# Kernel tuning notes

Measured on AMD Instinct MI355X. Metric: run time of the kernel, lower is better.

The kernel has to match this reference:

```python
import jax, jax.numpy as jnp
import numpy as np

EMBED = 512
HEADS = 8
DH = EMBED // HEADS  # 64
M = 256              # num_landmarks
ITERS = 6            # pinv iterations
SCALE = DH ** -0.5
RES_K = 33           # lucidrains residual_conv_kernel default


def _layer_norm(x, g, b, eps=1e-5):
    mu = jnp.mean(x, axis=-1, keepdims=True)
    var = jnp.mean((x - mu) ** 2, axis=-1, keepdims=True)
    return (x - mu) / jnp.sqrt(var + eps) * g + b


def _pinv_iter(x, iters=ITERS):
    # Moore-Penrose iterative pseudo-inverse (lucidrains nystrom-attention)
    abs_x = jnp.abs(x)
    denom = jnp.max(abs_x.sum(-1)) * jnp.max(abs_x.sum(-2))
    z = jnp.swapaxes(x, -1, -2) / denom
    I = jnp.eye(x.shape[-1], dtype=x.dtype)
    for _ in range(iters):
        xz = x @ z
        z = 0.25 * z @ (13 * I - xz @ (15 * I - xz @ (7 * I - xz)))
    return z


def _dwconv2d(x, w, b):
    # x: [B,C,H,W], w: [C,1,kh,kw] depthwise, SAME padding (odd kernels == k//2)
    out = jax.lax.conv_general_dilated(x, w, (1, 1), 'SAME',
                                       dimension_numbers=('NCHW', 'OIHW', 'NCHW'),
                                       feature_group_count=x.shape[1])
    return out + b[None, :, None, None]


def _nystrom_attn(x, Wqkv, Wo, bo, res_w):
    # x: [B, n, EMBED]; pad at FRONT so n divisible by M (matches F.pad(..., padding, 0) semantics)
    b, n, _ = x.shape
    pad = (M - n % M) % M
    x = jnp.pad(x, ((0, 0), (pad, 0), (0, 0)))
    npad = n + pad
    qkv = x @ Wqkv.T                               # [b, npad, 3*EMBED]
    q, k, v = jnp.split(qkv, 3, axis=-1)
    to_heads = lambda t: t.reshape(b, npad, HEADS, DH).transpose(0, 2, 1, 3)  # bhnd
    q, k, v = to_heads(q), to_heads(k), to_heads(v)
    q = q * SCALE
    l = npad // M
    q_land = q.reshape(b, HEADS, M, l, DH).mean(3)  # [b,h,M,d]
    k_land = k.reshape(b, HEADS, M, l, DH).mean(3)
    s1 = jnp.einsum('bhnd,bhmd->bhnm', q, k_land)
    s2 = jnp.einsum('bhmd,bhld->bhml', q_land, k_land)
    s3 = jnp.einsum('bhmd,bhnd->bhmn', q_land, k)
    a1 = jax.nn.softmax(s1, -1)
    a2 = jax.nn.softmax(s2, -1)
    a3 = jax.nn.softmax(s3, -1)
    a2_inv = _pinv_iter(a2)
    out = a1 @ (a2_inv @ (a3 @ v))                 # [b,h,npad,d]
    # residual depthwise conv over v: channels=heads, spatial=(npad, DH), kernel (33,1)
    res = jax.lax.conv_general_dilated(v, res_w, (1, 1), 'SAME',
                                       dimension_numbers=('NCHW', 'OIHW', 'NCHW'),
                                       feature_group_count=HEADS)
    out = out + res
    out = out.transpose(0, 2, 1, 3).reshape(b, npad, EMBED)
    out = out @ Wo.T + bo
    return out[:, -n:]                             # drop front padding


def setup_inputs() -> dict:
    key = jax.random.key(0)
    ks = jax.random.split(key, 32)
    s = 0.02
    inp = {}
    inp['data'] = jax.random.normal(ks[0], (4, 4096, 1536), jnp.float32)
    inp['W1'] = jax.random.normal(ks[1], (EMBED, 1536), jnp.float32) * s
    inp['b1'] = jnp.zeros((EMBED,), jnp.float32)
    inp['cls_token'] = jax.random.normal(ks[2], (1, 1, EMBED), jnp.float32)
    for li, base in ((1, 3), (2, 9)):
        inp[f'ln{li}_g'] = jnp.ones((EMBED,), jnp.float32)
        inp[f'ln{li}_b'] = jnp.zeros((EMBED,), jnp.float32)
        inp[f'Wqkv{li}'] = jax.random.normal(ks[base], (3 * EMBED, EMBED), jnp.float32) * s
        inp[f'Wo{li}'] = jax.random.normal(ks[base + 1], (EMBED, EMBED), jnp.float32) * s
        inp[f'bo{li}'] = jnp.zeros((EMBED,), jnp.float32)
        inp[f'res{li}'] = jax.random.normal(ks[base + 2], (HEADS, 1, RES_K, 1), jnp.float32) * s
    inp['pw7'] = jax.random.normal(ks[15], (EMBED, 1, 7, 7), jnp.float32) * s
    inp['pb7'] = jnp.zeros((EMBED,), jnp.float32)
    inp['pw5'] = jax.random.normal(ks[16], (EMBED, 1, 5, 5), jnp.float32) * s
    inp['pb5'] = jnp.zeros((EMBED,), jnp.float32)
    inp['pw3'] = jax.random.normal(ks[17], (EMBED, 1, 3, 3), jnp.float32) * s
    inp['pb3'] = jnp.zeros((EMBED,), jnp.float32)
    inp['lnf_g'] = jnp.ones((EMBED,), jnp.float32)
    inp['lnf_b'] = jnp.zeros((EMBED,), jnp.float32)
    inp['W2'] = jax.random.normal(ks[18], (2, EMBED), jnp.float32) * s
    inp['b2'] = jnp.zeros((2,), jnp.float32)
    return inp


def reference(data, W1, b1, cls_token, ln1_g, ln1_b, Wqkv1, Wo1, bo1, res1,
              ln2_g, ln2_b, Wqkv2, Wo2, bo2, res2,
              pw7, pb7, pw5, pb5, pw3, pb3, lnf_g, lnf_b, W2, b2):
    h = jax.nn.relu(data @ W1.T + b1)              # [B, N, EMBED]
    B, N, C = h.shape
    grid = int(np.ceil(np.sqrt(N)))
    add = grid * grid - N
    if add > 0:
        h = jnp.concatenate([h, h[:, :add]], axis=1)
    cls = jnp.broadcast_to(cls_token, (B, 1, C))
    h = jnp.concatenate([cls, h], axis=1)          # [B, 1+grid^2, C]
    # TransLayer 1
    h = h + _nystrom_attn(_layer_norm(h, ln1_g, ln1_b), Wqkv1, Wo1, bo1, res1)
    # PPEG
    cls_t, feat = h[:, :1], h[:, 1:]
    cnn = feat.transpose(0, 2, 1).reshape(B, C, grid, grid)
    x = _dwconv2d(cnn, pw7, pb7) + cnn + _dwconv2d(cnn, pw5, pb5) + _dwconv2d(cnn, pw3, pb3)
    feat = x.reshape(B, C, grid * grid).transpose(0, 2, 1)
    h = jnp.concatenate([cls_t, feat], axis=1)
    # TransLayer 2
    h = h + _nystrom_attn(_layer_norm(h, ln2_g, ln2_b), Wqkv2, Wo2, bo2, res2)
    h = _layer_norm(h, lnf_g, lnf_b)
    cls_feat = h[:, 0]
    logits = cls_feat @ W2.T + b2
    Y_prob = jax.nn.softmax(logits, -1)
    Y_hat = jnp.argmax(Y_prob, -1)
    return logits, Y_prob, Y_hat
```

## Files before the change

### kernel.cpp

```cpp
#include <hip/hip_runtime.h>
#include <math.h>

#define EMBED 512
#define HEADS 8
#define DH 64
#define MM 256
#define LSEG 17
#define NPAD 4352
#define NTOK 4097
#define N0 4096
#define BATCH 4
#define CIN 1536
#define QSCALE 0.125f
#define BH 32
#define NSEG 17

typedef float fp32x4 __attribute__((ext_vector_type(4)));
typedef short bf16x8 __attribute__((ext_vector_type(8)));
typedef short bf16x4 __attribute__((ext_vector_type(4)));
typedef unsigned short ushort_t;

__device__ __forceinline__ unsigned short f2bf(float f) {
  unsigned int u = __float_as_uint(f);
  u += 0x7fffu + ((u >> 16) & 1u);
  return (unsigned short)(u >> 16);
}
__device__ __forceinline__ float bf2f(unsigned short u) {
  return __uint_as_float((unsigned)u << 16);
}

__device__ __forceinline__ float block_sum(float v, float* red) {
  #pragma unroll
  for (int o = 1; o < 64; o <<= 1) v += __shfl_xor(v, o);
  int lane = threadIdx.x & 63, wid = threadIdx.x >> 6;
  if (lane == 0) red[wid] = v;
  __syncthreads();
  float r = red[0] + red[1] + red[2] + red[3];
  __syncthreads();
  return r;
}
__device__ __forceinline__ float block_max(float v, float* red) {
  #pragma unroll
  for (int o = 1; o < 64; o <<= 1) v = fmaxf(v, __shfl_xor(v, o));
  int lane = threadIdx.x & 63, wid = threadIdx.x >> 6;
  if (lane == 0) red[wid] = v;
  __syncthreads();
  float r = fmaxf(fmaxf(red[0], red[1]), fmaxf(red[2], red[3]));
  __syncthreads();
  return r;
}

__global__ __launch_bounds__(256) void gemm_abt(
    const float* __restrict__ A, const float* __restrict__ W,
    int Mrows, int Ncols, int K, const float* __restrict__ bias,
    float* __restrict__ out0, float* __restrict__ out1, float* __restrict__ out2,
    int mode)
{
  __shared__ unsigned short As[64][40];
  __shared__ unsigned short Ws[64][40];
  int tid = threadIdx.x;
  int lane = tid & 63;
  int wv = tid >> 6;
  int rowBase = blockIdx.y * 64, colBase = blockIdx.x * 64;
  int quad = lane >> 4;
  int l15 = lane & 15;
  int sr = tid >> 2;
  int skc = (tid & 3) * 8;

  fp32x4 acc[4] = {fp32x4{0,0,0,0}, fp32x4{0,0,0,0}, fp32x4{0,0,0,0}, fp32x4{0,0,0,0}};

  for (int kb = 0; kb < K; kb += 32) {
    __syncthreads();
    {
      int grow = rowBase + sr;
      float va[8];
      if (grow < Mrows) {
        const float4* p = (const float4*)&A[(size_t)grow * K + kb + skc];
        float4 v0 = p[0], v1 = p[1];
        va[0]=v0.x; va[1]=v0.y; va[2]=v0.z; va[3]=v0.w;
        va[4]=v1.x; va[5]=v1.y; va[6]=v1.z; va[7]=v1.w;
      } else {
        #pragma unroll
        for (int j = 0; j < 8; j++) va[j] = 0.f;
      }
      bf16x8 pk;
      #pragma unroll
      for (int j = 0; j < 8; j++) pk[j] = (short)f2bf(va[j]);
      *(bf16x8*)&As[sr][skc] = pk;
    }
    {
      int gcol = colBase + sr;
      const float4* p = (const float4*)&W[(size_t)gcol * K + kb + skc];
      float4 v0 = p[0], v1 = p[1];
      float vb[8] = {v0.x, v0.y, v0.z, v0.w, v1.x, v1.y, v1.z, v1.w};
      bf16x8 pk;
      #pragma unroll
      for (int j = 0; j < 8; j++) pk[j] = (short)f2bf(vb[j]);
      *(bf16x8*)&Ws[sr][skc] = pk;
    }
    __syncthreads();
    bf16x8 aF = *(const bf16x8*)&As[wv * 16 + l15][quad * 8];
    #pragma unroll
    for (int ns = 0; ns < 4; ns++) {
      bf16x8 bF = *(const bf16x8*)&Ws[ns * 16 + l15][quad * 8];
      acc[ns] = __builtin_amdgcn_mfma_f32_16x16x32_bf16(aF, bF, acc[ns], 0, 0, 0);
    }
  }

  #pragma unroll
  for (int ns = 0; ns < 4; ns++) {
    int col = colBase + ns * 16 + l15;
    #pragma unroll
    for (int i = 0; i < 4; i++) {
      int row = rowBase + wv * 16 + quad * 4 + i;
      if (row >= Mrows) continue;
      float v = acc[ns][i];
      if (mode == 0) {
        v += bias[col];
        v = fmaxf(v, 0.f);
        int b = row / N0, n = row % N0;
        out0[((size_t)b * NTOK + 1 + n) * EMBED + col] = v;
      } else if (mode == 1) {
        int b = row / NPAD, n = row % NPAD;
        int sec = col / EMBED;
        int hh = (col % EMBED) / DH;
        int d = col & 63;
        float* dst = (sec == 0) ? out0 : ((sec == 1) ? out1 : out2);
        if (sec == 0) v *= QSCALE;
        dst[(((size_t)b * HEADS + hh) * NPAD + n) * DH + d] = v;
      } else if (mode == 2) {
        v += bias[col];
        out0[(size_t)row * EMBED + col] += v;
      } else {
        v += bias[col];
        float full = out0[(size_t)row * EMBED + col] + v;
        out0[(size_t)row * EMBED + col] = full;
        int b = row / NTOK, t = row % NTOK;
        if (t > 0) out1[((size_t)b * N0 + (t - 1)) * EMBED + col] = full;
      }
    }
  }
}

#define BSWZ(n, k) ((((k) + (((n) >> 3) & 3) * 8)) & 31)
__global__ __launch_bounds__(256) void gemm_nn_bf16(
    const unsigned short* __restrict__ A, const unsigned short* __restrict__ B,
    unsigned short* __restrict__ C,
    int Nsize, float beta, float sgn, float gamma, int transOut)
{
  __shared__ unsigned short As[64][40];
  __shared__ unsigned short BsT[64][40];
  int batch = blockIdx.z;
  const unsigned short* Ab = A + (size_t)batch * MM * MM;
  const unsigned short* Bb = B + (size_t)batch * MM * Nsize;
  unsigned short* Cb = C + (size_t)batch * MM * Nsize;
  int tid = threadIdx.x;
  int lane = tid & 63, wv = tid >> 6, quad = lane >> 4, l15 = lane & 15;
  int rowBase = blockIdx.y * 64, colBase = blockIdx.x * 64;
  int asr = tid >> 2, ask = (tid & 3) * 8;
  int bkr = tid >> 3;
  int bnc = (tid & 7) * 8;
  fp32x4 acc[4] = {fp32x4{0,0,0,0}, fp32x4{0,0,0,0}, fp32x4{0,0,0,0}, fp32x4{0,0,0,0}};

  for (int kb = 0; kb < MM; kb += 32) {
    __syncthreads();
    *(bf16x8*)&As[asr][ask] =
        *(const bf16x8*)&Ab[(size_t)(rowBase + asr) * MM + kb + ask];
    {
      bf16x8 vb = *(const bf16x8*)&Bb[(size_t)(kb + bkr) * Nsize + colBase + bnc];
      #pragma unroll
      for (int j = 0; j < 8; j++) {
        int n = bnc + j;
        BsT[n][BSWZ(n, bkr)] = (unsigned short)vb[j];
      }
    }
    __syncthreads();
    bf16x8 aF = *(const bf16x8*)&As[wv * 16 + l15][quad * 8];
    #pragma unroll
    for (int ct = 0; ct < 4; ct++) {
      int n = ct * 16 + l15;
      bf16x8 bF = *(const bf16x8*)&BsT[n][BSWZ(n, quad * 8)];
      acc[ct] = __builtin_amdgcn_mfma_f32_16x16x32_bf16(aF, bF, acc[ct], 0, 0, 0);
    }
  }

  #pragma unroll
  for (int ct = 0; ct < 4; ct++) {
    int col = colBase + ct * 16 + l15;
    #pragma unroll
    for (int i = 0; i < 4; i++) {
      int row = rowBase + wv * 16 + quad * 4 + i;
      float v = sgn * acc[ct][i];
      if (beta != 0.f) v += beta * bf2f(Ab[(size_t)row * MM + col]);
      v *= gamma;
      if (transOut == 0) Cb[(size_t)row * Nsize + col] = f2bf(v);
      else               Cb[(size_t)col * MM + row] = f2bf(v);
    }
  }
}

__global__ void cls_kernel(const float* __restrict__ cls, float* __restrict__ h) {
  int t = blockIdx.x * blockDim.x + threadIdx.x;
  if (t >= BATCH * EMBED) return;
  int b = t / EMBED, c = t % EMBED;
  h[(size_t)b * NTOK * EMBED + c] = cls[c];
}

__global__ void zero_pad_kernel(float* __restrict__ xpad) {
  int t = blockIdx.x * blockDim.x + threadIdx.x;
  const int per = 255 * EMBED;
  if (t >= BATCH * per) return;
  int b = t / per, r = t % per;
  xpad[(size_t)b * NPAD * EMBED + r] = 0.f;
}

__global__ __launch_bounds__(256) void ln_pad_kernel(
    const float* __restrict__ h, const float* __restrict__ g,
    const float* __restrict__ be, float* __restrict__ xpad)
{
  __shared__ float red[4];
  int row = blockIdx.x;
  int b = row / NTOK, j = row % NTOK;
  const float* x = h + (size_t)row * EMBED;
  int tid = threadIdx.x;
  float v0 = x[tid], v1 = x[tid + 256];
  float mu = block_sum(v0 + v1, red) * (1.f / 512.f);
  float d0 = v0 - mu, d1 = v1 - mu;
  float var = block_sum(d0 * d0 + d1 * d1, red) * (1.f / 512.f);
  float inv = 1.f / sqrtf(var + 1e-5f);
  float* o = xpad + ((size_t)b * NPAD + 255 + j) * EMBED;
  o[tid]       = d0 * inv * g[tid]       + be[tid];
  o[tid + 256] = d1 * inv * g[tid + 256] + be[tid + 256];
}

__global__ __launch_bounds__(256) void landmarks_kernel(
    const float* __restrict__ q, const float* __restrict__ k,
    float* __restrict__ qland, float* __restrict__ kland)
{
  int bh = blockIdx.y;
  int m = blockIdx.x * 4 + (threadIdx.x >> 6);
  int d = threadIdx.x & 63;
  const float* qb = q + (size_t)bh * NPAD * DH;
  const float* kb = k + (size_t)bh * NPAD * DH;
  float sq = 0.f, sk = 0.f;
  int base = m * LSEG;
  #pragma unroll
  for (int t = 0; t < LSEG; t++) {
    sq += qb[(size_t)(base + t) * DH + d];
    sk += kb[(size_t)(base + t) * DH + d];
  }
  qland[((size_t)bh * MM + m) * DH + d] = sq * (1.f / LSEG);
  kland[((size_t)bh * MM + m) * DH + d] = sk * (1.f / LSEG);
}

__global__ __launch_bounds__(256) void s2_softmax_kernel(
    const float* __restrict__ qland, const float* __restrict__ kland,
    unsigned short* __restrict__ a2)
{
  __shared__ float qrow[64];
  __shared__ float red[4];
  int bh = blockIdx.y, m = blockIdx.x, tid = threadIdx.x;
  if (tid < 64) qrow[tid] = qland[((size_t)bh * MM + m) * DH + tid];
  __syncthreads();
  const float* kb = kland + (size_t)bh * MM * DH + (size_t)tid * DH;
  float s = 0.f;
  #pragma unroll 16
  for (int d = 0; d < 64; d++) s += qrow[d] * kb[d];
  float mx = block_max(s, red);
  float e = __expf(s - mx);
  float tot = block_sum(e, red);
  a2[((size_t)bh * MM + m) * MM + tid] = f2bf(e / tot);
}

__global__ void init_denom_kernel(float* __restrict__ denoms) {
  if (threadIdx.x < 2) denoms[threadIdx.x] = 0.f;
}

__global__ __launch_bounds__(256) void denom_kernel(
    const unsigned short* __restrict__ a2, float* __restrict__ denoms)
{
  __shared__ float red[4];
  int bh = blockIdx.x, tid = threadIdx.x;
  const unsigned short* A = a2 + (size_t)bh * MM * MM;
  float rs = 0.f, cs = 0.f;
  for (int j = 0; j < MM; j++) rs += bf2f(A[(size_t)tid * MM + j]);
  for (int i = 0; i < MM; i++) cs += bf2f(A[(size_t)i * MM + tid]);
  float mr = block_max(rs, red);
  float mc = block_max(cs, red);
  if (tid == 0) {
    atomicMax((int*)&denoms[0], __float_as_int(mr));
    atomicMax((int*)&denoms[1], __float_as_int(mc));
  }
}

__global__ void z0_kernel(const unsigned short* __restrict__ a2,
                          const float* __restrict__ denoms,
                          unsigned short* __restrict__ z)
{
  int bh = blockIdx.z;
  int i = blockIdx.y * 4 + threadIdx.y;
  int j = blockIdx.x * 64 + threadIdx.x;
  float denom = denoms[0] * denoms[1];
  z[((size_t)bh * MM + i) * MM + j] = f2bf(bf2f(a2[((size_t)bh * MM + j) * MM + i]) / denom);
}

__global__ __launch_bounds__(256) void a3v_part_mfma(
    const float* __restrict__ qland, const float* __restrict__ k,
    const float* __restrict__ v, float* __restrict__ Opart,
    float* __restrict__ mpart, float* __restrict__ lpart)
{
  __shared__ __align__(16) unsigned short qs[64][40];
  __shared__ __align__(16) unsigned short ks[256][72];
  __shared__ __align__(16) unsigned short vt[64][72];
  int tid = threadIdx.x;
  int lane = tid & 63, wv = tid >> 6, quad = lane >> 4, l15 = lane & 15;
  int bh = blockIdx.y;
  int ltile = blockIdx.x & 3;
  int seg = blockIdx.x >> 2;
  int l0 = ltile * 64;
  int key0 = seg * 256;
  const float* qb = qland + (size_t)bh * MM * DH;
  const float* kb = k + (size_t)bh * NPAD * DH;
  const float* vb = v + (size_t)bh * NPAD * DH;

  {
    int sr = tid >> 2, dc = (tid & 3) * 16;
    const float4* p = (const float4*)&qb[(size_t)(l0 + sr) * DH + dc];
    float4 v0 = p[0], v1 = p[1], v2 = p[2], v3 = p[3];
    float va[16] = {v0.x,v0.y,v0.z,v0.w, v1.x,v1.y,v1.z,v1.w,
                    v2.x,v2.y,v2.z,v2.w, v3.x,v3.y,v3.z,v3.w};
    bf16x8 p0, p1;
    #pragma unroll
    for (int j = 0; j < 8; j++) { p0[j] = (short)f2bf(va[j]); p1[j] = (short)f2bf(va[8 + j]); }
    *(bf16x8*)&qs[sr][dc] = p0;
    *(bf16x8*)&qs[sr][dc + 8] = p1;
  }
  #pragma unroll
  for (int i = 0; i < 16; i++) {
    int idx = i * 1024 + tid * 4;
    int r = idx >> 6, c = idx & 63;
    float4 vv = *(const float4*)&kb[(size_t)(key0 + r) * DH + c];
    bf16x4 pk = { (short)f2bf(vv.x), (short)f2bf(vv.y), (short)f2bf(vv.z), (short)f2bf(vv.w) };
    *(bf16x4*)&ks[r][c] = pk;
  }
  __syncthreads();

  fp32x4 sacc[16];
  #pragma unroll
  for (int ct = 0; ct < 16; ct++) sacc[ct] = fp32x4{0,0,0,0};
  bf16x8 aF0 = *(const bf16x8*)&qs[wv * 16 + l15][quad * 8];
  bf16x8 aF1 = *(const bf16x8*)&qs[wv * 16 + l15][32 + quad * 8];
  #pragma unroll
  for (int ct = 0; ct < 16; ct++) {
    bf16x8 b0 = *(const bf16x8*)&ks[ct * 16 + l15][quad * 8];
    bf16x8 b1 = *(const bf16x8*)&ks[ct * 16 + l15][32 + quad * 8];
    sacc[ct] = __builtin_amdgcn_mfma_f32_16x16x32_bf16(aF0, b0, sacc[ct], 0, 0, 0);
    sacc[ct] = __builtin_amdgcn_mfma_f32_16x16x32_bf16(aF1, b1, sacc[ct], 0, 0, 0);
  }

  float mrow[4], lrow[4];
  #pragma unroll
  for (int i = 0; i < 4; i++) {
    float m = -3.0e38f;
    #pragma unroll
    for (int ct = 0; ct < 16; ct++) m = fmaxf(m, sacc[ct][i]);
    #pragma unroll
    for (int o = 1; o < 16; o <<= 1) m = fmaxf(m, __shfl_xor(m, o));
    float s = 0.f;
    #pragma unroll
    for (int ct = 0; ct < 16; ct++) {
      float e = __expf(sacc[ct][i] - m);
      sacc[ct][i] = e;
      s += e;
    }
    #pragma unroll
    for (int o = 1; o < 16; o <<= 1) s += __shfl_xor(s, o);
    mrow[i] = m;
    lrow[i] = s;
  }
  __syncthreads();
  unsigned short* P = &ks[0][0];
  #pragma unroll
  for (int ct = 0; ct < 16; ct++)
    #pragma unroll
    for (int i = 0; i < 4; i++)
      P[(size_t)(wv * 16 + quad * 4 + i) * 264 + ct * 16 + l15] = f2bf(sacc[ct][i]);
  __syncthreads();

  fp32x4 oacc[4] = {fp32x4{0,0,0,0}, fp32x4{0,0,0,0}, fp32x4{0,0,0,0}, fp32x4{0,0,0,0}};
  int dh = tid & 63, kgrp = tid >> 6;
  for (int ch = 0; ch < 4; ch++) {
    if (ch) __syncthreads();
    {
      int kbase = kgrp * 16;
      #pragma unroll
      for (int g = 0; g < 4; g++) {
        short pk[4];
        #pragma unroll
        for (int r = 0; r < 4; r++)
          pk[r] = (short)f2bf(vb[(size_t)(key0 + ch * 64 + kbase + g * 4 + r) * DH + dh]);
        *(bf16x4*)&vt[dh][kbase + g * 4] = *(bf16x4*)pk;
      }
    }
    __syncthreads();
    #pragma unroll
    for (int ks2 = 0; ks2 < 2; ks2++) {
      bf16x8 aP = *(const bf16x8*)&P[(size_t)(wv * 16 + l15) * 264 + ch * 64 + ks2 * 32 + quad * 8];
      #pragma unroll
      for (int ct = 0; ct < 4; ct++) {
        bf16x8 bV = *(const bf16x8*)&vt[ct * 16 + l15][ks2 * 32 + quad * 8];
        oacc[ct] = __builtin_amdgcn_mfma_f32_16x16x32_bf16(aP, bV, oacc[ct], 0, 0, 0);
      }
    }
  }

  size_t base = ((size_t)seg * BH + bh) * MM + l0;
  #pragma unroll
  for (int ct = 0; ct < 4; ct++)
    #pragma unroll
    for (int i = 0; i < 4; i++) {
      int row = wv * 16 + quad * 4 + i;
      Opart[(base + row) * DH + ct * 16 + l15] = oacc[ct][i];
    }
  if (l15 == 0) {
    #pragma unroll
    for (int i = 0; i < 4; i++) {
      int row = wv * 16 + quad * 4 + i;
      mpart[base + row] = mrow[i];
      lpart[base + row] = lrow[i];
    }
  }
}

__global__ __launch_bounds__(256) void a3v_merge_kernel(
    const float* __restrict__ Opart, const float* __restrict__ mpart,
    const float* __restrict__ lpart, unsigned short* __restrict__ kv)
{
  int bh = blockIdx.y;
  int lbase = blockIdx.x * 64;
  int d = threadIdx.x & 63, lsub = threadIdx.x >> 6;
  for (int li = lsub; li < 64; li += 4) {
    int lm = lbase + li;
    float M = -3.0e38f;
    #pragma unroll
    for (int s = 0; s < NSEG; s++)
      M = fmaxf(M, mpart[((size_t)s * BH + bh) * MM + lm]);
    float L = 0.f, O = 0.f;
    #pragma unroll
    for (int s = 0; s < NSEG; s++) {
      size_t idx = ((size_t)s * BH + bh) * MM + lm;
      float w = __expf(mpart[idx] - M);
      L += lpart[idx] * w;
      O += Opart[idx * DH + d] * w;
    }
    kv[((size_t)bh * MM + lm) * DH + d] = f2bf(O / L);
  }
}

__global__ __launch_bounds__(256, 2) void attn1_mfma(
    const float* __restrict__ q, const float* __restrict__ kland,
    const unsigned short* __restrict__ kv2T, const float* __restrict__ v,
    const float* __restrict__ resw, float* __restrict__ attn)
{
  __shared__ __align__(16) unsigned short qs[64][40];
  __shared__ __align__(16) unsigned short klp[256][72];
  __shared__ __align__(16) unsigned short kvs[64][264];
  __shared__ float wsm[33];
  int tid = threadIdx.x;
  int lane = tid & 63, wv = tid >> 6, quad = lane >> 4, l15 = lane & 15;
  int bh = blockIdx.y, b = bh >> 3, hh = bh & 7;
  int n0 = 255 + blockIdx.x * 64;
  const float* qb  = q + (size_t)bh * NPAD * DH;
  const float* klb = kland + (size_t)bh * MM * DH;
  const unsigned short* kvb = kv2T + (size_t)bh * DH * MM;
  const float* vb  = v + (size_t)bh * NPAD * DH;
  if (tid < 33) wsm[tid] = resw[hh * 33 + tid];

  {
    int sr = tid >> 2, dc = (tid & 3) * 16;
    int g = n0 + sr; if (g > NPAD - 1) g = NPAD - 1;
    const float4* p = (const float4*)&qb[(size_t)g * DH + dc];
    float4 v0 = p[0], v1 = p[1], v2 = p[2], v3 = p[3];
    float va[16] = {v0.x,v0.y,v0.z,v0.w, v1.x,v1.y,v1.z,v1.w,
                    v2.x,v2.y,v2.z,v2.w, v3.x,v3.y,v3.z,v3.w};
    bf16x8 p0, p1;
    #pragma unroll
    for (int j = 0; j < 8; j++) { p0[j] = (short)f2bf(va[j]); p1[j] = (short)f2bf(va[8 + j]); }
    *(bf16x8*)&qs[sr][dc] = p0;
    *(bf16x8*)&qs[sr][dc + 8] = p1;
  }
  #pragma unroll
  for (int i = 0; i < 16; i++) {
    int idx = i * 1024 + tid * 4;
    int r = idx >> 6, c = idx & 63;
    float4 vv = *(const float4*)&klb[(size_t)r * DH + c];
    bf16x4 pk = { (short)f2bf(vv.x), (short)f2bf(vv.y), (short)f2bf(vv.z), (short)f2bf(vv.w) };
    *(bf16x4*)&klp[r][c] = pk;
  }
  #pragma unroll
  for (int i = 0; i < 8; i++) {
    int idx = i * 2048 + tid * 8;
    int r = idx >> 8, c = idx & 255;
    *(bf16x8*)&kvs[r][c] = *(const bf16x8*)&kvb[(size_t)r * MM + c];
  }
  __syncthreads();

  fp32x4 sacc[16];
  #pragma unroll
  for (int ct = 0; ct < 16; ct++) sacc[ct] = fp32x4{0,0,0,0};
  bf16x8 aF0 = *(const bf16x8*)&qs[wv * 16 + l15][quad * 8];
  bf16x8 aF1 = *(const bf16x8*)&qs[wv * 16 + l15][32 + quad * 8];
  #pragma unroll
  for (int ct = 0; ct < 16; ct++) {
    bf16x8 b0 = *(const bf16x8*)&klp[ct * 16 + l15][quad * 8];
    bf16x8 b1 = *(const bf16x8*)&klp[ct * 16 + l15][32 + quad * 8];
    sacc[ct] = __builtin_amdgcn_mfma_f32_16x16x32_bf16(aF0, b0, sacc[ct], 0, 0, 0);
    sacc[ct] = __builtin_amdgcn_mfma_f32_16x16x32_bf16(aF1, b1, sacc[ct], 0, 0, 0);
  }
  #pragma unroll
  for (int i = 0; i < 4; i++) {
    float m = -3.0e38f;
    #pragma unroll
    for (int ct = 0; ct < 16; ct++) m = fmaxf(m, sacc[ct][i]);
    #pragma unroll
    for (int o = 1; o < 16; o <<= 1) m = fmaxf(m, __shfl_xor(m, o));
    float s = 0.f;
    #pragma unroll
    for (int ct = 0; ct < 16; ct++) {
      float e = __expf(sacc[ct][i] - m);
      sacc[ct][i] = e;
      s += e;
    }
    #pragma unroll
    for (int o = 1; o < 16; o <<= 1) s += __shfl_xor(s, o);
    float inv = 1.f / s;
    #pragma unroll
    for (int ct = 0; ct < 16; ct++) sacc[ct][i] *= inv;
  }
  __syncthreads();
  unsigned short* P = &klp[0][0];
  #pragma unroll
  for (int ct = 0; ct < 16; ct++)
    #pragma unroll
    for (int i = 0; i < 4; i++)
      P[(size_t)(wv * 16 + quad * 4 + i) * 264 + ct * 16 + l15] = f2bf(sacc[ct][i]);
  __syncthreads();

  fp32x4 oacc[4] = {fp32x4{0,0,0,0}, fp32x4{0,0,0,0}, fp32x4{0,0,0,0}, fp32x4{0,0,0,0}};
  #pragma unroll
  for (int ks = 0; ks < 8; ks++) {
    bf16x8 aP = *(const bf16x8*)&P[(size_t)(wv * 16 + l15) * 264 + ks * 32 + quad * 8];
    #pragma unroll
    for (int ct = 0; ct < 4; ct++) {
      bf16x8 bV = *(const bf16x8*)&kvs[ct * 16 + l15][ks * 32 + quad * 8];
      oacc[ct] = __builtin_amdgcn_mfma_f32_16x16x32_bf16(aP, bV, oacc[ct], 0, 0, 0);
    }
  }
  __syncthreads();
  float* vwin = (float*)&kvs[0][0];
  #pragma unroll
  for (int i = 0; i < 6; i++) {
    int r = i * 16 + (tid >> 4), c = (tid & 15) * 4;
    int g = n0 - 16 + r;
    float4 vv;
    if (g <= NPAD - 1) vv = *(const float4*)&vb[(size_t)g * DH + c];
    else { vv.x = 0.f; vv.y = 0.f; vv.z = 0.f; vv.w = 0.f; }
    *(float4*)&vwin[r * 68 + c] = vv;
  }
  __syncthreads();
  #pragma unroll
  for (int ct = 0; ct < 4; ct++) {
    int c = ct * 16 + l15;
    #pragma unroll
    for (int i = 0; i < 4; i++) {
      int rl = wv * 16 + quad * 4 + i;
      int n = n0 + rl;
      if (n > NPAD - 1) continue;
      float ca = 0.f;
      #pragma unroll 11
      for (int t = 0; t < 33; t++) ca += vwin[(rl + t) * 68 + c] * wsm[t];
      attn[((size_t)b * NTOK + (n - 255)) * EMBED + hh * DH + c] = oacc[ct][i] + ca;
    }
  }
}

__global__ void prep_wcomb_kernel(
    const float* __restrict__ pw7, const float* __restrict__ pw5,
    const float* __restrict__ pw3, const float* __restrict__ pb7,
    const float* __restrict__ pb5, const float* __restrict__ pb3,
    float* __restrict__ wcomb, float* __restrict__ biasc)
{
  int i = blockIdx.x * blockDim.x + threadIdx.x;
  if (i < EMBED * 49) {
    int c = i / 49, tap = i % 49;
    int ky = tap / 7, kx = tap % 7;
    float v = pw7[c * 49 + tap];
    if (ky >= 1 && ky <= 5 && kx >= 1 && kx <= 5) v += pw5[c * 25 + (ky - 1) * 5 + (kx - 1)];
    if (ky >= 2 && ky <= 4 && kx >= 2 && kx <= 4) v += pw3[c * 9 + (ky - 2) * 3 + (kx - 2)];
    if (ky == 3 && kx == 3) v += 1.f;
    wcomb[tap * EMBED + c] = v;
  }
  if (i < EMBED) biasc[i] = pb7[i] + pb5[i] + pb3[i];
}

__global__ __launch_bounds__(256) void dwconv_kernel(
    const float* __restrict__ tmp, const float* __restrict__ wcomb,
    const float* __restrict__ biasc, float* __restrict__ h)
{
  __shared__ float4 wsm[49][32];
  int tx = threadIdx.x;
  int ty = threadIdx.y;
  int cb = blockIdx.x * 128;
  int c = cb + tx * 4;
  int b = blockIdx.z;
  int n = blockIdx.y * 8 + ty;
  int y = n >> 6, x = n & 63;
  int tid = ty * 32 + tx;
  for (int i = tid; i < 49 * 32; i += 256) {
    int tap = i >> 5, g = i & 31;
    wsm[tap][g] = *(const float4*)&wcomb[tap * EMBED + cb + g * 4];
  }
  __syncthreads();
  const float* src = tmp + (size_t)b * N0 * EMBED;
  float4 acc = *(const float4*)&biasc[c];
  #pragma unroll
  for (int ky = 0; ky < 7; ky++) {
    int yy = y + ky - 3;
    if (yy < 0 || yy >= 64) continue;
    #pragma unroll
    for (int kx = 0; kx < 7; kx++) {
      int xx = x + kx - 3;
      if (xx < 0 || xx >= 64) continue;
      float4 vv = *(const float4*)&src[((size_t)yy * 64 + xx) * EMBED + c];
      float4 w = wsm[ky * 7 + kx][tx];
      acc.x += vv.x * w.x;
      acc.y += vv.y * w.y;
      acc.z += vv.z * w.z;
      acc.w += vv.w * w.w;
    }
  }
  *(float4*)&h[((size_t)b * NTOK + 1 + n) * EMBED + c] = acc;
}

__global__ __launch_bounds__(256) void final_kernel(
    const float* __restrict__ h, const float* __restrict__ g,
    const float* __restrict__ be, const float* __restrict__ W2,
    const float* __restrict__ b2, float* __restrict__ out)
{
  __shared__ float red[4];
  int b = blockIdx.x, tid = threadIdx.x;
  const float* x = h + (size_t)b * NTOK * EMBED;
  float v0 = x[tid], v1 = x[tid + 256];
  float mu = block_sum(v0 + v1, red) * (1.f / 512.f);
  float d0 = v0 - mu, d1 = v1 - mu;
  float var = block_sum(d0 * d0 + d1 * d1, red) * (1.f / 512.f);
  float inv = 1.f / sqrtf(var + 1e-5f);
  float xn0 = d0 * inv * g[tid] + be[tid];
  float xn1 = d1 * inv * g[tid + 256] + be[tid + 256];
  float l0 = block_sum(xn0 * W2[tid] + xn1 * W2[tid + 256], red);
  float l1 = block_sum(xn0 * W2[512 + tid] + xn1 * W2[512 + tid + 256], red);
  if (tid == 0) {
    l0 += b2[0]; l1 += b2[1];
    out[b * 2 + 0] = l0;
    out[b * 2 + 1] = l1;
    float mx = fmaxf(l0, l1);
    float e0 = expf(l0 - mx), e1 = expf(l1 - mx);
    float s = e0 + e1;
    out[8 + b * 2 + 0] = e0 / s;
    out[8 + b * 2 + 1] = e1 / s;
    out[16 + b] = (l1 > l0) ? 1.f : 0.f;
  }
}

extern "C" void kernel_launch(void* const* d_in, const int* in_sizes, int n_in,
                              void* d_out, int out_size, void* d_ws, size_t ws_size,
                              hipStream_t stream)
{
  const float* data = (const float*)d_in[0];
  const float* W1   = (const float*)d_in[1];
  const float* b1   = (const float*)d_in[2];
  const float* cls  = (const float*)d_in[3];
  const float* lng[2]  = {(const float*)d_in[4],  (const float*)d_in[10]};
  const float* lnb[2]  = {(const float*)d_in[5],  (const float*)d_in[11]};
  const float* Wqkv[2] = {(const float*)d_in[6],  (const float*)d_in[12]};
  const float* Wo[2]   = {(const float*)d_in[7],  (const float*)d_in[13]};
  const float* bo[2]   = {(const float*)d_in[8],  (const float*)d_in[14]};
  const float* resw[2] = {(const float*)d_in[9],  (const float*)d_in[15]};
  const float* pw7 = (const float*)d_in[16];
  const float* pb7 = (const float*)d_in[17];
  const float* pw5 = (const float*)d_in[18];
  const float* pb5 = (const float*)d_in[19];
  const float* pw3 = (const float*)d_in[20];
  const float* pb3 = (const float*)d_in[21];
  const float* lnfg = (const float*)d_in[22];
  const float* lnfb = (const float*)d_in[23];
  const float* W2  = (const float*)d_in[24];
  const float* b2  = (const float*)d_in[25];

  float* ws = (float*)d_ws;
  size_t off = 0;
  auto alloc = [&](size_t n) { float* p = ws + off; off += n; return p; };
  float* hbuf  = alloc((size_t)BATCH * NTOK * EMBED);
  float* xpad  = alloc((size_t)BATCH * NPAD * EMBED);
  float* qbuf  = alloc((size_t)BH * NPAD * DH);
  float* kbuf  = alloc((size_t)BH * NPAD * DH);
  float* vbuf  = alloc((size_t)BH * NPAD * DH);
  float* qland = alloc((size_t)BH * MM * DH);
  float* kland = alloc((size_t)BH * MM * DH);
  float* a2f   = alloc((size_t)BH * MM * MM);
  float* za    = alloc((size_t)BH * MM * MM);
  float* zb    = alloc((size_t)BH * MM * MM);
  float* xzb   = alloc((size_t)BH * MM * MM);
  float* t1b   = alloc((size_t)BH * MM * MM);
  float* t2b   = alloc((size_t)BH * MM * MM);
  float* kvb   = alloc((size_t)BH * MM * DH);
  float* kv2b  = alloc((size_t)BH * MM * DH);
  float* wcomb = alloc(49 * EMBED);
  float* biasc = alloc(EMBED);
  float* denoms = alloc(64);
  float* mpart = alloc((size_t)NSEG * BH * MM);
  float* lpart = alloc((size_t)NSEG * BH * MM);
  float* attn = xpad;
  float* Opart = za;

  unsigned short* a2B  = (unsigned short*)a2f;
  unsigned short* zaB  = (unsigned short*)za;
  unsigned short* zbB  = (unsigned short*)zb;
  unsigned short* xzB  = (unsigned short*)xzb;
  unsigned short* t1B  = (unsigned short*)t1b;
  unsigned short* t2B  = (unsigned short*)t2b;
  unsigned short* kvB  = (unsigned short*)kvb;
  unsigned short* kv2B = (unsigned short*)kv2b;

  gemm_abt<<<dim3(EMBED / 64, (BATCH * N0) / 64), 256, 0, stream>>>(
      data, W1, BATCH * N0, EMBED, CIN, b1, hbuf, nullptr, nullptr, 0);
  cls_kernel<<<dim3((BATCH * EMBED + 255) / 256), 256, 0, stream>>>(cls, hbuf);

  for (int layer = 0; layer < 2; layer++) {
    ln_pad_kernel<<<dim3(BATCH * NTOK), 256, 0, stream>>>(hbuf, lng[layer], lnb[layer], xpad);
    zero_pad_kernel<<<dim3((BATCH * 255 * EMBED + 255) / 256), 256, 0, stream>>>(xpad);
    gemm_abt<<<dim3((3 * EMBED) / 64, (BATCH * NPAD) / 64), 256, 0, stream>>>(
        xpad, Wqkv[layer], BATCH * NPAD, 3 * EMBED, EMBED, nullptr, qbuf, kbuf, vbuf, 1);
    landmarks_kernel<<<dim3(MM / 4, BH), 256, 0, stream>>>(qbuf, kbuf, qland, kland);
    s2_softmax_kernel<<<dim3(MM, BH), 256, 0, stream>>>(qland, kland, a2B);
    init_denom_kernel<<<1, 64, 0, stream>>>(denoms);
    denom_kernel<<<dim3(BH), 256, 0, stream>>>(a2B, denoms);

    a3v_part_mfma<<<dim3(4 * NSEG, BH), 256, 0, stream>>>(
        qland, kbuf, vbuf, Opart, mpart, lpart);
    a3v_merge_kernel<<<dim3(MM / 64, BH), 256, 0, stream>>>(Opart, mpart, lpart, kvB);

    z0_kernel<<<dim3(MM / 64, MM / 4, BH), dim3(64, 4), 0, stream>>>(a2B, denoms, zaB);
    unsigned short* zin = zaB;
    unsigned short* zout = zbB;
    for (int it = 0; it < 6; it++) {
      gemm_nn_bf16<<<dim3(4, 4, BH), 256, 0, stream>>>(a2B, zin, xzB, MM, 0.f, 1.f, 1.f, 0);
      gemm_nn_bf16<<<dim3(4, 4, BH), 256, 0, stream>>>(xzB, xzB, t1B, MM, 7.f, -1.f, 1.f, 0);
      gemm_nn_bf16<<<dim3(4, 4, BH), 256, 0, stream>>>(xzB, t1B, t2B, MM, 15.f, -1.f, 1.f, 0);
      gemm_nn_bf16<<<dim3(4, 4, BH), 256, 0, stream>>>(zin, t2B, zout, MM, 13.f, -1.f, 0.25f, 0);
      unsigned short* t = zin; zin = zout; zout = t;
    }
    gemm_nn_bf16<<<dim3(1, 4, BH), 256, 0, stream>>>(zin, kvB, kv2B, DH, 0.f, 1.f, 1.f, 1);
    attn1_mfma<<<dim3((NTOK + 63) / 64, BH), 256, 0, stream>>>(
        qbuf, kland, kv2B, vbuf, resw[layer], attn);
    gemm_abt<<<dim3(EMBED / 64, (BATCH * NTOK + 63) / 64), 256, 0, stream>>>(
        attn, Wo[layer], BATCH * NTOK, EMBED, EMBED, bo[layer], hbuf,
        (layer == 0) ? qbuf : nullptr, nullptr, (layer == 0) ? 3 : 2);

    if (layer == 0) {
      prep_wcomb_kernel<<<dim3((EMBED * 49 + 255) / 256), 256, 0, stream>>>(
          pw7, pw5, pw3, pb7, pb5, pb3, wcomb, biasc);
      dwconv_kernel<<<dim3(EMBED / 128, N0 / 8, BATCH), dim3(32, 8), 0, stream>>>(
          qbuf, wcomb, biasc, hbuf);
    }
  }

  final_kernel<<<dim3(BATCH), 256, 0, stream>>>(hbuf, lnfg, lnfb, W2, b2, (float*)d_out);
}
```

Baseline: 1.703 ms.

## Store activations and weights in bf16, widen GEMM tiles, keep dual-layout pinv buffers

Converts the input data and weights to bf16 once up front, and stores q/k/v, the padded LN output, attention output and partial results as bf16 instead of fp32. This halves global memory traffic and removes the per-tile fp32-to-bf16 conversion inside the GEMMs. gemm_abt now computes 64x128 tiles. The pinv GEMMs write both row-major and column-major copies so B operands load without a transposing scatter into shared memory. The costs are extra conversion passes over the large input, doubled output writes in the pinv loop, and more bf16 rounding of intermediates.

After: 1.589 ms. -6.7%, faster.

```diff
diff --git a/kernel.cpp b/kernel.cpp
--- a/kernel.cpp
+++ b/kernel.cpp
@@ -18,7 +18,7 @@
 typedef float fp32x4 __attribute__((ext_vector_type(4)));
 typedef short bf16x8 __attribute__((ext_vector_type(8)));
 typedef short bf16x4 __attribute__((ext_vector_type(4)));
-typedef unsigned short ushort_t;
+typedef unsigned short u16;
 
 __device__ __forceinline__ unsigned short f2bf(float f) {
   unsigned int u = __float_as_uint(f);
@@ -50,136 +50,123 @@
   return r;
 }
 
+__global__ void f2bf_kernel(const float* __restrict__ in, u16* __restrict__ out, int n) {
+  int t = (blockIdx.x * 256 + threadIdx.x) * 8;
+  if (t >= n) return;
+  float4 a = *(const float4*)&in[t];
+  float4 b = *(const float4*)&in[t + 4];
+  bf16x8 pk;
+  pk[0]=(short)f2bf(a.x); pk[1]=(short)f2bf(a.y); pk[2]=(short)f2bf(a.z); pk[3]=(short)f2bf(a.w);
+  pk[4]=(short)f2bf(b.x); pk[5]=(short)f2bf(b.y); pk[6]=(short)f2bf(b.z); pk[7]=(short)f2bf(b.w);
+  *(bf16x8*)&out[t] = pk;
+}
+
 __global__ __launch_bounds__(256) void gemm_abt(
-    const float* __restrict__ A, const float* __restrict__ W,
+    const u16* __restrict__ A, const u16* __restrict__ W,
     int Mrows, int Ncols, int K, const float* __restrict__ bias,
-    float* __restrict__ out0, float* __restrict__ out1, float* __restrict__ out2,
+    float* __restrict__ fout, float* __restrict__ fout2,
+    u16* __restrict__ uo0, u16* __restrict__ uo1, u16* __restrict__ uo2,
     int mode)
 {
-  __shared__ unsigned short As[64][40];
-  __shared__ unsigned short Ws[64][40];
+  __shared__ u16 As[64][40];
+  __shared__ u16 Ws[128][40];
   int tid = threadIdx.x;
   int lane = tid & 63;
   int wv = tid >> 6;
-  int rowBase = blockIdx.y * 64, colBase = blockIdx.x * 64;
+  int rowBase = blockIdx.y * 64, colBase = blockIdx.x * 128;
   int quad = lane >> 4;
   int l15 = lane & 15;
   int sr = tid >> 2;
   int skc = (tid & 3) * 8;
 
-  fp32x4 acc[4] = {fp32x4{0,0,0,0}, fp32x4{0,0,0,0}, fp32x4{0,0,0,0}, fp32x4{0,0,0,0}};
+  fp32x4 acc[8];
+  #pragma unroll
+  for (int i = 0; i < 8; i++) acc[i] = fp32x4{0,0,0,0};
 
   for (int kb = 0; kb < K; kb += 32) {
     __syncthreads();
     {
       int grow = rowBase + sr;
-      float va[8];
-      if (grow < Mrows) {
-        const float4* p = (const float4*)&A[(size_t)grow * K + kb + skc];
-        float4 v0 = p[0], v1 = p[1];
-        va[0]=v0.x; va[1]=v0.y; va[2]=v0.z; va[3]=v0.w;
-        va[4]=v1.x; va[5]=v1.y; va[6]=v1.z; va[7]=v1.w;
-      } else {
-        #pragma unroll
-        for (int j = 0; j < 8; j++) va[j] = 0.f;
-      }
-      bf16x8 pk;
-      #pragma unroll
-      for (int j = 0; j < 8; j++) pk[j] = (short)f2bf(va[j]);
-      *(bf16x8*)&As[sr][skc] = pk;
-    }
-    {
-      int gcol = colBase + sr;
-      const float4* p = (const float4*)&W[(size_t)gcol * K + kb + skc];
-      float4 v0 = p[0], v1 = p[1];
-      float vb[8] = {v0.x, v0.y, v0.z, v0.w, v1.x, v1.y, v1.z, v1.w};
-      bf16x8 pk;
-      #pragma unroll
-      for (int j = 0; j < 8; j++) pk[j] = (short)f2bf(vb[j]);
-      *(bf16x8*)&Ws[sr][skc] = pk;
+      bf16x8 av;
+      if (grow < Mrows) av = *(const bf16x8*)&A[(size_t)grow * K + kb + skc];
+      else { bf16x8 z = {0,0,0,0,0,0,0,0}; av = z; }
+      *(bf16x8*)&As[sr][skc] = av;
+    }
+    #pragma unroll
+    for (int h = 0; h < 2; h++) {
+      int r = sr + h * 64;
+      *(bf16x8*)&Ws[r][skc] =
+          *(const bf16x8*)&W[(size_t)(colBase + r) * K + kb + skc];
     }
     __syncthreads();
     bf16x8 aF = *(const bf16x8*)&As[wv * 16 + l15][quad * 8];
     #pragma unroll
-    for (int ns = 0; ns < 4; ns++) {
-      bf16x8 bF = *(const bf16x8*)&Ws[ns * 16 + l15][quad * 8];
-      acc[ns] = __builtin_amdgcn_mfma_f32_16x16x32_bf16(aF, bF, acc[ns], 0, 0, 0);
-    }
-  }
-
-  #pragma unroll
-  for (int ns = 0; ns < 4; ns++) {
-    int col = colBase + ns * 16 + l15;
+    for (int ct = 0; ct < 8; ct++) {
+      bf16x8 bF = *(const bf16x8*)&Ws[ct * 16 + l15][quad * 8];
+      acc[ct] = __builtin_amdgcn_mfma_f32_16x16x32_bf16(aF, bF, acc[ct], 0, 0, 0);
+    }
+  }
+
+  #pragma unroll
+  for (int ct = 0; ct < 8; ct++) {
+    int col = colBase + ct * 16 + l15;
     #pragma unroll
     for (int i = 0; i < 4; i++) {
       int row = rowBase + wv * 16 + quad * 4 + i;
       if (row >= Mrows) continue;
-      float v = acc[ns][i];
+      float v = acc[ct][i];
       if (mode == 0) {
         v += bias[col];
         v = fmaxf(v, 0.f);
         int b = row / N0, n = row % N0;
-        out0[((size_t)b * NTOK + 1 + n) * EMBED + col] = v;
+        fout[((size_t)b * NTOK + 1 + n) * EMBED + col] = v;
       } else if (mode == 1) {
         int b = row / NPAD, n = row % NPAD;
         int sec = col / EMBED;
         int hh = (col % EMBED) / DH;
         int d = col & 63;
-        float* dst = (sec == 0) ? out0 : ((sec == 1) ? out1 : out2);
+        u16* dst = (sec == 0) ? uo0 : ((sec == 1) ? uo1 : uo2);
         if (sec == 0) v *= QSCALE;
-        dst[(((size_t)b * HEADS + hh) * NPAD + n) * DH + d] = v;
+        dst[(((size_t)b * HEADS + hh) * NPAD + n) * DH + d] = f2bf(v);
       } else if (mode == 2) {
         v += bias[col];
-        out0[(size_t)row * EMBED + col] += v;
+        fout[(size_t)row * EMBED + col] += v;
       } else {
         v += bias[col];
-        float full = out0[(size_t)row * EMBED + col] + v;
-        out0[(size_t)row * EMBED + col] = full;
+        float full = fout[(size_t)row * EMBED + col] + v;
+        fout[(size_t)row * EMBED + col] = full;
         int b = row / NTOK, t = row % NTOK;
-        if (t > 0) out1[((size_t)b * N0 + (t - 1)) * EMBED + col] = full;
+        if (t > 0) fout2[((size_t)b * N0 + (t - 1)) * EMBED + col] = full;
       }
     }
   }
 }
 
-#define BSWZ(n, k) ((((k) + (((n) >> 3) & 3) * 8)) & 31)
-__global__ __launch_bounds__(256) void gemm_nn_bf16(
-    const unsigned short* __restrict__ A, const unsigned short* __restrict__ B,
-    unsigned short* __restrict__ C,
-    int Nsize, float beta, float sgn, float gamma, int transOut)
-{
-  __shared__ unsigned short As[64][40];
-  __shared__ unsigned short BsT[64][40];
+__global__ __launch_bounds__(256) void gemm_nn2(
+    const u16* __restrict__ A, const u16* __restrict__ Bc,
+    u16* __restrict__ Cr, u16* __restrict__ Cc,
+    int Nsize, float beta, float sgn, float gamma)
+{
+  __shared__ u16 As[64][40];
+  __shared__ u16 Bs[64][40];
   int batch = blockIdx.z;
-  const unsigned short* Ab = A + (size_t)batch * MM * MM;
-  const unsigned short* Bb = B + (size_t)batch * MM * Nsize;
-  unsigned short* Cb = C + (size_t)batch * MM * Nsize;
+  const u16* Ab = A + (size_t)batch * MM * MM;
+  const u16* Bb = Bc + (size_t)batch * MM * Nsize;
   int tid = threadIdx.x;
   int lane = tid & 63, wv = tid >> 6, quad = lane >> 4, l15 = lane & 15;
   int rowBase = blockIdx.y * 64, colBase = blockIdx.x * 64;
-  int asr = tid >> 2, ask = (tid & 3) * 8;
-  int bkr = tid >> 3;
-  int bnc = (tid & 7) * 8;
+  int sr = tid >> 2, skc = (tid & 3) * 8;
   fp32x4 acc[4] = {fp32x4{0,0,0,0}, fp32x4{0,0,0,0}, fp32x4{0,0,0,0}, fp32x4{0,0,0,0}};
 
   for (int kb = 0; kb < MM; kb += 32) {
     __syncthreads();
-    *(bf16x8*)&As[asr][ask] =
-        *(const bf16x8*)&Ab[(size_t)(rowBase + asr) * MM + kb + ask];
-    {
-      bf16x8 vb = *(const bf16x8*)&Bb[(size_t)(kb + bkr) * Nsize + colBase + bnc];
-      #pragma unroll
-      for (int j = 0; j < 8; j++) {
-        int n = bnc + j;
-        BsT[n][BSWZ(n, bkr)] = (unsigned short)vb[j];
-      }
-    }
+    *(bf16x8*)&As[sr][skc] = *(const bf16x8*)&Ab[(size_t)(rowBase + sr) * MM + kb + skc];
+    *(bf16x8*)&Bs[sr][skc] = *(const bf16x8*)&Bb[(size_t)(colBase + sr) * MM + kb + skc];
     __syncthreads();
     bf16x8 aF = *(const bf16x8*)&As[wv * 16 + l15][quad * 8];
     #pragma unroll
     for (int ct = 0; ct < 4; ct++) {
-      int n = ct * 16 + l15;
-      bf16x8 bF = *(const bf16x8*)&BsT[n][BSWZ(n, quad * 8)];
+      bf16x8 bF = *(const bf16x8*)&Bs[ct * 16 + l15][quad * 8];
       acc[ct] = __builtin_amdgcn_mfma_f32_16x16x32_bf16(aF, bF, acc[ct], 0, 0, 0);
     }
   }
@@ -193,8 +180,9 @@
       float v = sgn * acc[ct][i];
       if (beta != 0.f) v += beta * bf2f(Ab[(size_t)row * MM + col]);
       v *= gamma;
-      if (transOut == 0) Cb[(size_t)row * Nsize + col] = f2bf(v);
-      else               Cb[(size_t)col * MM + row] = f2bf(v);
+      u16 o = f2bf(v);
+      if (Cr) Cr[(size_t)batch * MM * Nsize + (size_t)row * Nsize + col] = o;
+      if (Cc) Cc[(size_t)batch * MM * Nsize + (size_t)col * MM + row] = o;
     }
   }
 }
@@ -206,17 +194,17 @@
   h[(size_t)b * NTOK * EMBED + c] = cls[c];
 }
 
-__global__ void zero_pad_kernel(float* __restrict__ xpad) {
+__global__ void zero_pad_kernel(u16* __restrict__ xpad) {
   int t = blockIdx.x * blockDim.x + threadIdx.x;
   const int per = 255 * EMBED;
   if (t >= BATCH * per) return;
   int b = t / per, r = t % per;
-  xpad[(size_t)b * NPAD * EMBED + r] = 0.f;
+  xpad[(size_t)b * NPAD * EMBED + r] = 0;
 }
 
 __global__ __launch_bounds__(256) void ln_pad_kernel(
     const float* __restrict__ h, const float* __restrict__ g,
-    const float* __restrict__ be, float* __restrict__ xpad)
+    const float* __restrict__ be, u16* __restrict__ xpad)
 {
   __shared__ float red[4];
   int row = blockIdx.x;
@@ -228,26 +216,26 @@
   float d0 = v0 - mu, d1 = v1 - mu;
   float var = block_sum(d0 * d0 + d1 * d1, red) * (1.f / 512.f);
   float inv = 1.f / sqrtf(var + 1e-5f);
-  float* o = xpad + ((size_t)b * NPAD + 255 + j) * EMBED;
-  o[tid]       = d0 * inv * g[tid]       + be[tid];
-  o[tid + 256] = d1 * inv * g[tid + 256] + be[tid + 256];
+  u16* o = xpad + ((size_t)b * NPAD + 255 + j) * EMBED;
+  o[tid]       = f2bf(d0 * inv * g[tid]       + be[tid]);
+  o[tid + 256] = f2bf(d1 * inv * g[tid + 256] + be[tid + 256]);
 }
 
 __global__ __launch_bounds__(256) void landmarks_kernel(
-    const float* __restrict__ q, const float* __restrict__ k,
+    const u16* __restrict__ q, const u16* __restrict__ k,
     float* __restrict__ qland, float* __restrict__ kland)
 {
   int bh = blockIdx.y;
   int m = blockIdx.x * 4 + (threadIdx.x >> 6);
   int d = threadIdx.x & 63;
-  const float* qb = q + (size_t)bh * NPAD * DH;
-  const float* kb = k + (size_t)bh * NPAD * DH;
+  const u16* qb = q + (size_t)bh * NPAD * DH;
+  const u16* kb = k + (size_t)bh * NPAD * DH;
   float sq = 0.f, sk = 0.f;
   int base = m * LSEG;
   #pragma unroll
   for (int t = 0; t < LSEG; t++) {
-    sq += qb[(size_t)(base + t) * DH + d];
-    sk += kb[(size_t)(base + t) * DH + d];
+    sq += bf2f(qb[(size_t)(base + t) * DH + d]);
+    sk += bf2f(kb[(size_t)(base + t) * DH + d]);
   }
   qland[((size_t)bh * MM + m) * DH + d] = sq * (1.f / LSEG);
   kland[((size_t)bh * MM + m) * DH + d] = sk * (1.f / LSEG);
@@ -255,7 +243,7 @@
 
 __global__ __launch_bounds__(256) void s2_softmax_kernel(
     const float* __restrict__ qland, const float* __restrict__ kland,
-    unsigned short* __restrict__ a2)
+    u16* __restrict__ a2)
 {
   __shared__ float qrow[64];
   __shared__ float red[4];
@@ -277,11 +265,11 @@
 }
 
 __global__ __launch_bounds__(256) void denom_kernel(
-    const unsigned short* __restrict__ a2, float* __restrict__ denoms)
+    const u16* __restrict__ a2, float* __restrict__ denoms)
 {
   __shared__ float red[4];
   int bh = blockIdx.x, tid = threadIdx.x;
-  const unsigned short* A = a2 + (size_t)bh * MM * MM;
+  const u16* A = a2 + (size_t)bh * MM * MM;
   float rs = 0.f, cs = 0.f;
   for (int j = 0; j < MM; j++) rs += bf2f(A[(size_t)tid * MM + j]);
   for (int i = 0; i < MM; i++) cs += bf2f(A[(size_t)i * MM + tid]);
@@ -293,25 +281,45 @@
   }
 }
 
-__global__ void z0_kernel(const unsigned short* __restrict__ a2,
-                          const float* __restrict__ denoms,
-                          unsigned short* __restrict__ z)
-{
-  int bh = blockIdx.z;
-  int i = blockIdx.y * 4 + threadIdx.y;
-  int j = blockIdx.x * 64 + threadIdx.x;
-  float denom = denoms[0] * denoms[1];
-  z[((size_t)bh * MM + i) * MM + j] = f2bf(bf2f(a2[((size_t)bh * MM + j) * MM + i]) / denom);
+__global__ __launch_bounds__(256) void z0_trans_kernel(
+    const u16* __restrict__ a2, const float* __restrict__ denoms,
+    u16* __restrict__ zr, u16* __restrict__ zc)
+{
+  __shared__ u16 tile[64][72];
+  int bh = blockIdx.z, i0 = blockIdx.y * 64, j0 = blockIdx.x * 64;
+  int tid = threadIdx.x;
+  float inv = 1.f / (denoms[0] * denoms[1]);
+  const u16* Ab = a2 + (size_t)bh * MM * MM;
+  #pragma unroll
+  for (int it = 0; it < 4; it++) {
+    int idx = it * 1024 + tid * 4;
+    int r = idx >> 6, c = idx & 63;
+    bf16x4 v = *(const bf16x4*)&Ab[(size_t)(i0 + r) * MM + j0 + c];
+    u16 o[4];
+    #pragma unroll
+    for (int j = 0; j < 4; j++) o[j] = f2bf(bf2f((unsigned short)v[j]) * inv);
+    *(bf16x4*)&zc[(size_t)bh * MM * MM + (size_t)(i0 + r) * MM + j0 + c] = *(bf16x4*)o;
+    #pragma unroll
+    for (int j = 0; j < 4; j++) tile[c + j][r] = o[j];
+  }
+  __syncthreads();
+  #pragma unroll
+  for (int it = 0; it < 4; it++) {
+    int idx = it * 1024 + tid * 4;
+    int r = idx >> 6, c = idx & 63;
+    u16 o[4] = {tile[r][c], tile[r][c + 1], tile[r][c + 2], tile[r][c + 3]};
+    *(bf16x4*)&zr[(size_t)bh * MM * MM + (size_t)(j0 + r) * MM + i0 + c] = *(bf16x4*)o;
+  }
 }
 
 __global__ __launch_bounds__(256) void a3v_part_mfma(
-    const float* __restrict__ qland, const float* __restrict__ k,
-    const float* __restrict__ v, float* __restrict__ Opart,
+    const float* __restrict__ qland, const u16* __restrict__ k,
+    const u16* __restrict__ v, u16* __restrict__ Opart,
     float* __restrict__ mpart, float* __restrict__ lpart)
 {
-  __shared__ __align__(16) unsigned short qs[64][40];
-  __shared__ __align__(16) unsigned short ks[256][72];
-  __shared__ __align__(16) unsigned short vt[64][72];
+  __shared__ __align__(16) u16 qs[64][40];
+  __shared__ __align__(16) u16 ks[256][72];
+  __shared__ __align__(16) u16 vt[64][72];
   int tid = threadIdx.x;
   int lane = tid & 63, wv = tid >> 6, quad = lane >> 4, l15 = lane & 15;
   int bh = blockIdx.y;
@@ -320,8 +328,8 @@
   int l0 = ltile * 64;
   int key0 = seg * 256;
   const float* qb = qland + (size_t)bh * MM * DH;
-  const float* kb = k + (size_t)bh * NPAD * DH;
-  const float* vb = v + (size_t)bh * NPAD * DH;
+  const u16* kb = k + (size_t)bh * NPAD * DH;
+  const u16* vb = v + (size_t)bh * NPAD * DH;
 
   {
     int sr = tid >> 2, dc = (tid & 3) * 16;
@@ -339,9 +347,7 @@
   for (int i = 0; i < 16; i++) {
     int idx = i * 1024 + tid * 4;
     int r = idx >> 6, c = idx & 63;
-    float4 vv = *(const float4*)&kb[(size_t)(key0 + r) * DH + c];
-    bf16x4 pk = { (short)f2bf(vv.x), (short)f2bf(vv.y), (short)f2bf(vv.z), (short)f2bf(vv.w) };
-    *(bf16x4*)&ks[r][c] = pk;
+    *(bf16x4*)&ks[r][c] = *(const bf16x4*)&kb[(size_t)(key0 + r) * DH + c];
   }
   __syncthreads();
 
@@ -379,7 +385,7 @@
     lrow[i] = s;
   }
   __syncthreads();
-  unsigned short* P = &ks[0][0];
+  u16* P = &ks[0][0];
   #pragma unroll
   for (int ct = 0; ct < 16; ct++)
     #pragma unroll
@@ -395,10 +401,10 @@
       int kbase = kgrp * 16;
       #pragma unroll
       for (int g = 0; g < 4; g++) {
-        short pk[4];
+        u16 pk[4];
         #pragma unroll
         for (int r = 0; r < 4; r++)
-          pk[r] = (short)f2bf(vb[(size_t)(key0 + ch * 64 + kbase + g * 4 + r) * DH + dh]);
+          pk[r] = vb[(size_t)(key0 + ch * 64 + kbase + g * 4 + r) * DH + dh];
         *(bf16x4*)&vt[dh][kbase + g * 4] = *(bf16x4*)pk;
       }
     }
@@ -420,7 +426,7 @@
     #pragma unroll
     for (int i = 0; i < 4; i++) {
       int row = wv * 16 + quad * 4 + i;
-      Opart[(base + row) * DH + ct * 16 + l15] = oacc[ct][i];
+      Opart[(base + row) * DH + ct * 16 + l15] = f2bf(oacc[ct][i]);
     }
   if (l15 == 0) {
     #pragma unroll
@@ -433,8 +439,8 @@
 }
 
 __global__ __launch_bounds__(256) void a3v_merge_kernel(
-    const float* __restrict__ Opart, const float* __restrict__ mpart,
-    const float* __restrict__ lpart, unsigned short* __restrict__ kv)
+    const u16* __restrict__ Opart, const float* __restrict__ mpart,
+    const float* __restrict__ lpart, u16* __restrict__ kvT)
 {
   int bh = blockIdx.y;
   int lbase = blockIdx.x * 64;
@@ -451,43 +457,36 @@
       size_t idx = ((size_t)s * BH + bh) * MM + lm;
       float w = __expf(mpart[idx] - M);
       L += lpart[idx] * w;
-      O += Opart[idx * DH + d] * w;
-    }
-    kv[((size_t)bh * MM + lm) * DH + d] = f2bf(O / L);
+      O += bf2f(Opart[idx * DH + d]) * w;
+    }
+    kvT[((size_t)bh * DH + d) * MM + lm] = f2bf(O / L);
   }
 }
 
 __global__ __launch_bounds__(256, 2) void attn1_mfma(
-    const float* __restrict__ q, const float* __restrict__ kland,
-    const unsigned short* __restrict__ kv2T, const float* __restrict__ v,
-    const float* __restrict__ resw, float* __restrict__ attn)
-{
-  __shared__ __align__(16) unsigned short qs[64][40];
-  __shared__ __align__(16) unsigned short klp[256][72];
-  __shared__ __align__(16) unsigned short kvs[64][264];
+    const u16* __restrict__ q, const float* __restrict__ kland,
+    const u16* __restrict__ kv2T, const u16* __restrict__ v,
+    const float* __restrict__ resw, u16* __restrict__ attn)
+{
+  __shared__ __align__(16) u16 qs[64][40];
+  __shared__ __align__(16) u16 klp[256][72];
+  __shared__ __align__(16) u16 kvs[64][264];
   __shared__ float wsm[33];
   int tid = threadIdx.x;
   int lane = tid & 63, wv = tid >> 6, quad = lane >> 4, l15 = lane & 15;
   int bh = blockIdx.y, b = bh >> 3, hh = bh & 7;
   int n0 = 255 + blockIdx.x * 64;
-  const float* qb  = q + (size_t)bh * NPAD * DH;
+  const u16* qb  = q + (size_t)bh * NPAD * DH;
   const float* klb = kland + (size_t)bh * MM * DH;
-  const unsigned short* kvb = kv2T + (size_t)bh * DH * MM;
-  const float* vb  = v + (size_t)bh * NPAD * DH;
+  const u16* kvb = kv2T + (size_t)bh * DH * MM;
+  const u16* vb  = v + (size_t)bh * NPAD * DH;
   if (tid < 33) wsm[tid] = resw[hh * 33 + tid];
 
   {
     int sr = tid >> 2, dc = (tid & 3) * 16;
     int g = n0 + sr; if (g > NPAD - 1) g = NPAD - 1;
-    const float4* p = (const float4*)&qb[(size_t)g * DH + dc];
-    float4 v0 = p[0], v1 = p[1], v2 = p[2], v3 = p[3];
-    float va[16] = {v0.x,v0.y,v0.z,v0.w, v1.x,v1.y,v1.z,v1.w,
-                    v2.x,v2.y,v2.z,v2.w, v3.x,v3.y,v3.z,v3.w};
-    bf16x8 p0, p1;
-    #pragma unroll
-    for (int j = 0; j < 8; j++) { p0[j] = (short)f2bf(va[j]); p1[j] = (short)f2bf(va[8 + j]); }
-    *(bf16x8*)&qs[sr][dc] = p0;
-    *(bf16x8*)&qs[sr][dc + 8] = p1;
+    *(bf16x8*)&qs[sr][dc]     = *(const bf16x8*)&qb[(size_t)g * DH + dc];
+    *(bf16x8*)&qs[sr][dc + 8] = *(const bf16x8*)&qb[(size_t)g * DH + dc + 8];
   }
   #pragma unroll
   for (int i = 0; i < 16; i++) {
@@ -538,7 +537,7 @@
     for (int ct = 0; ct < 16; ct++) sacc[ct][i] *= inv;
   }
   __syncthreads();
-  unsigned short* P = &klp[0][0];
+  u16* P = &klp[0][0];
   #pragma unroll
   for (int ct = 0; ct < 16; ct++)
     #pragma unroll
@@ -563,8 +562,11 @@
     int r = i * 16 + (tid >> 4), c = (tid & 15) * 4;
     int g = n0 - 16 + r;
     float4 vv;
-    if (g <= NPAD - 1) vv = *(const float4*)&vb[(size_t)g * DH + c];
-    else { vv.x = 0.f; vv.y = 0.f; vv.z = 0.f; vv.w = 0.f; }
+    if (g <= NPAD - 1) {
+      bf16x4 bv = *(const bf16x4*)&vb[(size_t)g * DH + c];
+      vv.x = bf2f((unsigned short)bv[0]); vv.y = bf2f((unsigned short)bv[1]);
+      vv.z = bf2f((unsigned short)bv[2]); vv.w = bf2f((unsigned short)bv[3]);
+    } else { vv.x = 0.f; vv.y = 0.f; vv.z = 0.f; vv.w = 0.f; }
     *(float4*)&vwin[r * 68 + c] = vv;
   }
   __syncthreads();
@@ -579,7 +581,7 @@
       float ca = 0.f;
       #pragma unroll 11
       for (int t = 0; t < 33; t++) ca += vwin[(rl + t) * 68 + c] * wsm[t];
-      attn[((size_t)b * NTOK + (n - 255)) * EMBED + hh * DH + c] = oacc[ct][i] + ca;
+      attn[((size_t)b * NTOK + (n - 255)) * EMBED + hh * DH + c] = f2bf(oacc[ct][i] + ca);
     }
   }
 }
@@ -700,78 +702,101 @@
   float* ws = (float*)d_ws;
   size_t off = 0;
   auto alloc = [&](size_t n) { float* p = ws + off; off += n; return p; };
-  float* hbuf  = alloc((size_t)BATCH * NTOK * EMBED);
-  float* xpad  = alloc((size_t)BATCH * NPAD * EMBED);
-  float* qbuf  = alloc((size_t)BH * NPAD * DH);
-  float* kbuf  = alloc((size_t)BH * NPAD * DH);
-  float* vbuf  = alloc((size_t)BH * NPAD * DH);
-  float* qland = alloc((size_t)BH * MM * DH);
-  float* kland = alloc((size_t)BH * MM * DH);
-  float* a2f   = alloc((size_t)BH * MM * MM);
-  float* za    = alloc((size_t)BH * MM * MM);
-  float* zb    = alloc((size_t)BH * MM * MM);
-  float* xzb   = alloc((size_t)BH * MM * MM);
-  float* t1b   = alloc((size_t)BH * MM * MM);
-  float* t2b   = alloc((size_t)BH * MM * MM);
-  float* kvb   = alloc((size_t)BH * MM * DH);
-  float* kv2b  = alloc((size_t)BH * MM * DH);
-  float* wcomb = alloc(49 * EMBED);
-  float* biasc = alloc(EMBED);
+  float* hbuf   = alloc((size_t)BATCH * NTOK * EMBED);
+  float* xpadf  = alloc((size_t)BATCH * NPAD * EMBED);
+  float* qbuff  = alloc((size_t)BH * NPAD * DH);
+  float* kbuff  = alloc((size_t)BH * NPAD * DH);
+  float* vbuff  = alloc((size_t)BH * NPAD * DH);
+  float* qland  = alloc((size_t)BH * MM * DH);
+  float* kland  = alloc((size_t)BH * MM * DH);
+  float* a2f    = alloc((size_t)BH * MM * MM / 2);
+  float* zaRf   = alloc((size_t)BH * MM * MM / 2);
+  float* zaCf   = alloc((size_t)BH * MM * MM / 2);
+  float* zbRf   = alloc((size_t)BH * MM * MM / 2);
+  float* zbCf   = alloc((size_t)BH * MM * MM / 2);
+  float* xzRf   = alloc((size_t)BH * MM * MM / 2);
+  float* xzCf   = alloc((size_t)BH * MM * MM / 2);
+  float* t1Cf   = alloc((size_t)BH * MM * MM / 2);
+  float* t2Cf   = alloc((size_t)BH * MM * MM / 2);
+  float* kvTf   = alloc((size_t)BH * MM * DH / 2);
+  float* kv2Tf  = alloc((size_t)BH * MM * DH / 2);
+  float* wqkvbf = alloc((size_t)2 * 3 * EMBED * EMBED / 2);
+  float* wobf   = alloc((size_t)2 * EMBED * EMBED / 2);
+  float* wcomb  = alloc(49 * EMBED);
+  float* biasc  = alloc(EMBED);
   float* denoms = alloc(64);
-  float* mpart = alloc((size_t)NSEG * BH * MM);
-  float* lpart = alloc((size_t)NSEG * BH * MM);
-  float* attn = xpad;
-  float* Opart = za;
-
-  unsigned short* a2B  = (unsigned short*)a2f;
-  unsigned short* zaB  = (unsigned short*)za;
-  unsigned short* zbB  = (unsigned short*)zb;
-  unsigned short* xzB  = (unsigned short*)xzb;
-  unsigned short* t1B  = (unsigned short*)t1b;
-  unsigned short* t2B  = (unsigned short*)t2b;
-  unsigned short* kvB  = (unsigned short*)kvb;
-  unsigned short* kv2B = (unsigned short*)kv2b;
-
-  gemm_abt<<<dim3(EMBED / 64, (BATCH * N0) / 64), 256, 0, stream>>>(
-      data, W1, BATCH * N0, EMBED, CIN, b1, hbuf, nullptr, nullptr, 0);
+  float* mpart  = alloc((size_t)NSEG * BH * MM);
+  float* lpart  = alloc((size_t)NSEG * BH * MM);
+
+  u16* xpadB = (u16*)xpadf;
+  u16* qB = (u16*)qbuff;
+  u16* kB = (u16*)kbuff;
+  u16* vB = (u16*)vbuff;
+  u16* a2B = (u16*)a2f;
+  u16* zaR = (u16*)zaRf; u16* zaC = (u16*)zaCf;
+  u16* zbR = (u16*)zbRf; u16* zbC = (u16*)zbCf;
+  u16* xzR = (u16*)xzRf; u16* xzC = (u16*)xzCf;
+  u16* t1C = (u16*)t1Cf; u16* t2C = (u16*)t2Cf;
+  u16* kvT = (u16*)kvTf; u16* kv2T = (u16*)kv2Tf;
+  u16* attnB = xpadB;
+  u16* OpartB = zaR;
+  u16* databf = (u16*)qbuff;
+  u16* W1bf = (u16*)vbuff;
+  u16* WqkvB[2] = {(u16*)wqkvbf, (u16*)wqkvbf + (size_t)3 * EMBED * EMBED};
+  u16* WoB[2]   = {(u16*)wobf,   (u16*)wobf + (size_t)EMBED * EMBED};
+  float* convtmp = qbuff;
+
+  int ndata = BATCH * N0 * CIN;
+  f2bf_kernel<<<dim3((ndata / 8 + 255) / 256), 256, 0, stream>>>(data, databf, ndata);
+  f2bf_kernel<<<dim3((EMBED * CIN / 8 + 255) / 256), 256, 0, stream>>>(W1, W1bf, EMBED * CIN);
+  for (int l = 0; l < 2; l++) {
+    f2bf_kernel<<<dim3((3 * EMBED * EMBED / 8 + 255) / 256), 256, 0, stream>>>(Wqkv[l], WqkvB[l], 3 * EMBED * EMBED);
+    f2bf_kernel<<<dim3((EMBED * EMBED / 8 + 255) / 256), 256, 0, stream>>>(Wo[l], WoB[l], EMBED * EMBED);
+  }
+
+  gemm_abt<<<dim3(EMBED / 128, (BATCH * N0) / 64), 256, 0, stream>>>(
+      databf, W1bf, BATCH * N0, EMBED, CIN, b1, hbuf, nullptr, nullptr, nullptr, nullptr, 0);
   cls_kernel<<<dim3((BATCH * EMBED + 255) / 256), 256, 0, stream>>>(cls, hbuf);
 
   for (int layer = 0; layer < 2; layer++) {
-    ln_pad_kernel<<<dim3(BATCH * NTOK), 256, 0, stream>>>(hbuf, lng[layer], lnb[layer], xpad);
-    zero_pad_kernel<<<dim3((BATCH * 255 * EMBED + 255) / 256), 256, 0, stream>>>(xpad);
-    gemm_abt<<<dim3((3 * EMBED) / 64, (BATCH * NPAD) / 64), 256, 0, stream>>>(
-        xpad, Wqkv[layer], BATCH * NPAD, 3 * EMBED, EMBED, nullptr, qbuf, kbuf, vbuf, 1);
-    landmarks_kernel<<<dim3(MM / 4, BH), 256, 0, stream>>>(qbuf, kbuf, qland, kland);
+    ln_pad_kernel<<<dim3(BATCH * NTOK), 256, 0, stream>>>(hbuf, lng[layer], lnb[layer], xpadB);
+    zero_pad_kernel<<<dim3((BATCH * 255 * EMBED + 255) / 256), 256, 0, stream>>>(xpadB);
+    gemm_abt<<<dim3((3 * EMBED) / 128, (BATCH * NPAD) / 64), 256, 0, stream>>>(
+        xpadB, WqkvB[layer], BATCH * NPAD, 3 * EMBED, EMBED, nullptr,
+        nullptr, nullptr, qB, kB, vB, 1);
+    landmarks_kernel<<<dim3(MM / 4, BH), 256, 0, stream>>>(qB, kB, qland, kland);
     s2_softmax_kernel<<<dim3(MM, BH), 256, 0, stream>>>(qland, kland, a2B);
     init_denom_kernel<<<1, 64, 0, stream>>>(denoms);
     denom_kernel<<<dim3(BH), 256, 0, stream>>>(a2B, denoms);
 
     a3v_part_mfma<<<dim3(4 * NSEG, BH), 256, 0, stream>>>(
-        qland, kbuf, vbuf, Opart, mpart, lpart);
-    a3v_merge_kernel<<<dim3(MM / 64, BH), 256, 0, stream>>>(Opart, mpart, lpart, kvB);
-
-    z0_kernel<<<dim3(MM / 64, MM / 4, BH), dim3(64, 4), 0, stream>>>(a2B, denoms, zaB);
-    unsigned short* zin = zaB;
-    unsigned short* zout = zbB;
+        qland, kB, vB, OpartB, mpart, lpart);
+    a3v_merge_kernel<<<dim3(MM / 64, BH), 256, 0, stream>>>(OpartB, mpart, lpart, kvT);
+
+    z0_trans_kernel<<<dim3(4, 4, BH), 256, 0, stream>>>(a2B, denoms, zaR, zaC);
+    u16 *zinR = zaR, *zinC = zaC, *zoutR = zbR, *zoutC = zbC;
     for (int it = 0; it < 6; it++) {
-      gemm_nn_bf16<<<dim3(4, 4, BH), 256, 0, stream>>>(a2B, zin, xzB, MM, 0.f, 1.f, 1.f, 0);
-      gemm_nn_bf16<<<dim3(4, 4, BH), 256, 0, stream>>>(xzB, xzB, t1B, MM, 7.f, -1.f, 1.f, 0);
-      gemm_nn_bf16<<<dim3(4, 4, BH), 256, 0, stream>>>(xzB, t1B, t2B, MM, 15.f, -1.f, 1.f, 0);
-      gemm_nn_bf16<<<dim3(4, 4, BH), 256, 0, stream>>>(zin, t2B, zout, MM, 13.f, -1.f, 0.25f, 0);
-      unsigned short* t = zin; zin = zout; zout = t;
-    }
-    gemm_nn_bf16<<<dim3(1, 4, BH), 256, 0, stream>>>(zin, kvB, kv2B, DH, 0.f, 1.f, 1.f, 1);
+      gemm_nn2<<<dim3(4, 4, BH), 256, 0, stream>>>(a2B, zinC, xzR, xzC, MM, 0.f, 1.f, 1.f);
+      gemm_nn2<<<dim3(4, 4, BH), 256, 0, stream>>>(xzR, xzC, nullptr, t1C, MM, 7.f, -1.f, 1.f);
+      gemm_nn2<<<dim3(4, 4, BH), 256, 0, stream>>>(xzR, t1C, nullptr, t2C, MM, 15.f, -1.f, 1.f);
+      gemm_nn2<<<dim3(4, 4, BH), 256, 0, stream>>>(zinR, t2C, zoutR, zoutC, MM, 13.f, -1.f, 0.25f);
+      u16* t;
+      t = zinR; zinR = zoutR; zoutR = t;
+      t = zinC; zinC = zoutC; zoutC = t;
+    }
+    gemm_nn2<<<dim3(1, 4, BH), 256, 0, stream>>>(zinR, kvT, nullptr, kv2T, DH, 0.f, 1.f, 1.f);
     attn1_mfma<<<dim3((NTOK + 63) / 64, BH), 256, 0, stream>>>(
-        qbuf, kland, kv2B, vbuf, resw[layer], attn);
-    gemm_abt<<<dim3(EMBED / 64, (BATCH * NTOK + 63) / 64), 256, 0, stream>>>(
-        attn, Wo[layer], BATCH * NTOK, EMBED, EMBED, bo[layer], hbuf,
-        (layer == 0) ? qbuf : nullptr, nullptr, (layer == 0) ? 3 : 2);
+        qB, kland, kv2T, vB, resw[layer], attnB);
+    gemm_abt<<<dim3(EMBED / 128, (BATCH * NTOK + 63) / 64), 256, 0, stream>>>(
+        attnB, WoB[layer], BATCH * NTOK, EMBED, EMBED, bo[layer], hbuf,
+        (layer == 0) ? convtmp : nullptr, nullptr, nullptr, nullptr,
+        (layer == 0) ? 3 : 2);
 
     if (layer == 0) {
       prep_wcomb_kernel<<<dim3((EMBED * 49 + 255) / 256), 256, 0, stream>>>(
           pw7, pw5, pw3, pb7, pb5, pb3, wcomb, biasc);
       dwconv_kernel<<<dim3(EMBED / 128, N0 / 8, BATCH), dim3(32, 8), 0, stream>>>(
-          qbuf, wcomb, biasc, hbuf);
+          convtmp, wcomb, biasc, hbuf);
     }
   }
 
```
